# Performance work log

Measured on AMD Instinct MI355X. Metric: run time of the kernel, lower is better.

Reference implementation:

```python
import jax, jax.numpy as jnp
import numpy as np

B, N_ATOMS = 64, 127            # graphs, atoms per graph (uniform)
L = N_ATOMS + 1                 # +1 cls token
D_MODEL, NHEAD, NUM_LAYERS, D_FF = 1024, 16, 8, 3072
HEAD_DIM = D_MODEL // NHEAD
MAX_TOKENS = 131                # 121 + 10
NEIGH_VOCAB = 14 + 3            # max_neighbors + 3
DIST_VOCAB = 83 + 3             # max_distance + 3
EPS = 1e-5


def _dist_bins():
    # short_cutoff=0.9, long_cutoff=5.0, precision=0.05; first 3 edges overridden
    b = np.arange(0.9 - 3 * 0.05, 5.0, 0.05)
    b[:3] = [-1.0, 0.0, 0.01]
    return jnp.asarray(b, jnp.float32)  # len 85 -> digitize indices in [0, 85]


def _layer_norm(x, g, b):
    m = jnp.mean(x, -1, keepdims=True)
    v = jnp.var(x, -1, keepdims=True)
    return (x - m) * jax.lax.rsqrt(v + EPS) * g + b


def setup_inputs() -> dict:
    key = jax.random.key(0)
    ks = jax.random.split(key, 16)
    s = 0.02
    z = jax.random.randint(ks[0], (B * N_ATOMS,), 0, 119)
    hgs = jax.random.randint(ks[1], (B * N_ATOMS,), 0, 15)
    pos = jax.random.normal(ks[2], (B * N_ATOMS, 3), jnp.float32) * 3.0
    batch = jnp.repeat(jnp.arange(B, dtype=jnp.int64), N_ATOMS)
    atoms_emb = (jax.random.normal(ks[3], (MAX_TOKENS, D_MODEL), jnp.float32) * s).at[0].set(0.0)  # padding_idx=0
    neigh_emb = (jax.random.normal(ks[4], (NEIGH_VOCAB, D_MODEL), jnp.float32) * s).at[0].set(0.0)
    dist_emb = jax.random.normal(ks[5], (DIST_VOCAB, NHEAD), jnp.float32) * s  # row 0 forced to -inf in reference
    Wqkv = jax.random.normal(ks[6], (D_MODEL, 3 * D_MODEL), jnp.float32) * s
    bqkv = jnp.zeros((3 * D_MODEL,), jnp.float32)
    Wo = jax.random.normal(ks[7], (D_MODEL, D_MODEL), jnp.float32) * s
    bo = jnp.zeros((D_MODEL,), jnp.float32)
    W1 = jax.random.normal(ks[8], (D_MODEL, D_FF), jnp.float32) * s
    b1f = jnp.zeros((D_FF,), jnp.float32)
    W2 = jax.random.normal(ks[9], (D_FF, D_MODEL), jnp.float32) * s
    b2f = jnp.zeros((D_MODEL,), jnp.float32)
    ln1_g = jnp.ones((D_MODEL,), jnp.float32); ln1_b = jnp.zeros((D_MODEL,), jnp.float32)
    ln2_g = jnp.ones((D_MODEL,), jnp.float32); ln2_b = jnp.zeros((D_MODEL,), jnp.float32)
    return dict(z=z, hgs=hgs, pos=pos, batch=batch, atoms_emb=atoms_emb, neigh_emb=neigh_emb,
                dist_emb=dist_emb, Wqkv=Wqkv, bqkv=bqkv, Wo=Wo, bo=bo,
                W1=W1, b1f=b1f, W2=W2, b2f=b2f,
                ln1_g=ln1_g, ln1_b=ln1_b, ln2_g=ln2_g, ln2_b=ln2_b)


def reference(z, hgs, pos, batch, atoms_emb, neigh_emb, dist_emb,
              Wqkv, bqkv, Wo, bo, W1, b1f, W2, b2f, ln1_g, ln1_b, ln2_g, ln2_b):
    # batch is uniform (N_ATOMS per graph, sorted), so per-graph batching == reshape
    zb = z.reshape(B, N_ATOMS).astype(jnp.int32) + 2
    hb = hgs.reshape(B, N_ATOMS).astype(jnp.int32) + 2
    atoms = jnp.concatenate([jnp.ones((B, 1), jnp.int32), zb], axis=1)        # cls token = 1
    neighbors = jnp.concatenate([jnp.zeros((B, 1), jnp.int32), hb], axis=1)   # cls neighbors = 0

    p = pos.reshape(B, N_ATOMS, 3)
    dist = jnp.sqrt(jnp.sum((p[:, None, :, :] - p[:, :, None, :]) ** 2, axis=-1))  # (B,n,n)
    didx = jnp.digitize(dist, _dist_bins()).astype(jnp.int32)                      # self-loop -> 2
    distances = jnp.ones((B, L, L), jnp.int32).at[:, 1:, 1:].set(didx)             # cls row/col = 1

    # neg_inf_idx=0 padding mask row (unused here since no padding -> indices >= 1)
    w_d = dist_emb.at[0].set(-jnp.inf)
    d_mask = w_d[distances].transpose(0, 3, 1, 2)  # (B, H, L, L)

    x = atoms_emb[atoms] + neigh_emb[neighbors]    # (B, L, D)
    scale = 1.0 / jnp.sqrt(jnp.float32(HEAD_DIM))
    for _ in range(NUM_LAYERS):  # shared weights + shared attention bias
        qkv = x @ Wqkv + bqkv
        q, k, v = jnp.split(qkv, 3, axis=-1)
        q = q.reshape(B, L, NHEAD, HEAD_DIM)
        k = k.reshape(B, L, NHEAD, HEAD_DIM)
        v = v.reshape(B, L, NHEAD, HEAD_DIM)
        scores = jnp.einsum('blhd,bmhd->bhlm', q, k) * scale + d_mask
        a = jax.nn.softmax(scores, axis=-1)
        o = jnp.einsum('bhlm,bmhd->blhd', a, v).reshape(B, L, D_MODEL) @ Wo + bo
        x = _layer_norm(x + o, ln1_g, ln1_b)                      # post-norm (norm_first=False)
        h = jax.nn.gelu(x @ W1 + b1f, approximate=False) @ W2 + b2f
        x = _layer_norm(x + h, ln2_g, ln2_b)
    return x[:, 0]  # cls embedding, (B, D_MODEL)
```

## Files before the change

### kernel.cpp

```cpp
#include <hip/hip_runtime.h>
#include <cstdint>
#include <math.h>

typedef unsigned short u16;
typedef __attribute__((ext_vector_type(4))) float f32x4;
typedef __attribute__((ext_vector_type(8))) __bf16 bf16x8;
typedef __attribute__((ext_vector_type(8))) short short8;

typedef __attribute__((address_space(1))) void g_void;
typedef __attribute__((address_space(3))) void l_void;

__device__ __forceinline__ u16 f2bf(float f) {
  uint32_t u = __builtin_bit_cast(uint32_t, f);
  u += 0x7FFFu + ((u >> 16) & 1u);
  return (u16)(u >> 16);
}
__device__ __forceinline__ float bf2f(u16 h) {
  uint32_t u = ((uint32_t)h) << 16;
  return __builtin_bit_cast(float, u);
}

__device__ __forceinline__ void gload16(const void* g, void* l) {
  __builtin_amdgcn_global_load_lds((g_void*)g, (l_void*)l, 16, 0, 0);
}

__device__ __forceinline__ float gelu_exact(float x) {
  float a = x * 0.70710678118654752f;
  float s = fabsf(a);
  float t = __builtin_amdgcn_rcpf(fmaf(0.3275911f, s, 1.0f));
  float p = fmaf(fmaf(fmaf(fmaf(1.061405429f, t, -1.453152027f), t, 1.421413741f), t,
                      -0.284496736f), t, 0.254829592f);
  p *= t;
  float e = __expf(-s * s);
  float er = fmaf(-p, e, 1.0f);
  er = copysignf(er, a);
  return 0.5f * x * (1.0f + er);
}

__global__ void transpose_w(const float* __restrict__ W, u16* __restrict__ Wt, int K, int N) {
  __shared__ float t[32][33];
  const int nb = blockIdx.x * 32, kb = blockIdx.y * 32;
  const int tx = threadIdx.x, ty = threadIdx.y;
#pragma unroll
  for (int i = 0; i < 32; i += 8)
    t[ty + i][tx] = W[(size_t)(kb + ty + i) * N + nb + tx];
  __syncthreads();
#pragma unroll
  for (int i = 0; i < 32; i += 8)
    Wt[(size_t)(nb + ty + i) * K + kb + tx] = f2bf(t[tx][ty + i]);
}

__global__ void embed_k(const int* __restrict__ z, const int* __restrict__ hgs,
                        const float* __restrict__ ae, const float* __restrict__ ne,
                        u16* __restrict__ xb) {
  const int row = blockIdx.x;
  const int b = row >> 7, tl = row & 127;
  int ia = 1, in_ = 0;
  if (tl > 0) { ia = z[b * 127 + tl - 1] + 2; in_ = hgs[b * 127 + tl - 1] + 2; }
  const float* ar = ae + (size_t)ia * 1024;
  const float* nr = ne + (size_t)in_ * 1024;
  for (int c = threadIdx.x; c < 1024; c += 256)
    xb[(size_t)row * 1024 + c] = f2bf(ar[c] + nr[c]);
}

__global__ void mask_k(const float* __restrict__ pos, const float* __restrict__ demb,
                       u16* __restrict__ mask) {
  __shared__ float edges[85];
  __shared__ float dh[86 * 16];
  const int bq = blockIdx.x;
  const int b = bq >> 7, lq = bq & 127;
  const int lk = threadIdx.x;
  if (lk < 85) {
    double e = 0.75 + 0.05 * (double)lk;
    float ef = (float)e;
    if (lk == 0) ef = -1.0f; else if (lk == 1) ef = 0.0f; else if (lk == 2) ef = 0.01f;
    edges[lk] = ef;
  }
  for (int i = lk; i < 86 * 16; i += 128) {
    float v = demb[i];
    if (i < 16) v = -INFINITY;
    dh[i] = v;
  }
  __syncthreads();
  int c;
  if (lq == 0 || lk == 0) {
    c = 1;
  } else {
    const float* pi = pos + ((size_t)b * 127 + lq - 1) * 3;
    const float* pj = pos + ((size_t)b * 127 + lk - 1) * 3;
    const float dx = pi[0] - pj[0], dy = pi[1] - pj[1], dz = pi[2] - pj[2];
    const float d = sqrtf(dx * dx + dy * dy + dz * dz);
    int cnt = 0;
#pragma unroll
    for (int k2 = 0; k2 < 85; ++k2) cnt += (edges[k2] <= d) ? 1 : 0;
    c = cnt;
  }
#pragma unroll
  for (int h = 0; h < 16; ++h)
    mask[(((size_t)b * 16 + h) * 128 + lq) * 128 + lk] = f2bf(dh[c * 16 + h]);
}

template <int MODE, int RT>
__launch_bounds__(256, 2)
__global__ void gemmP(const u16* __restrict__ A, const u16* __restrict__ Bt,
                      const float* __restrict__ bias,
                      u16* __restrict__ O0, u16* __restrict__ O1, u16* __restrict__ O2,
                      int N, int K) {
  extern __shared__ char lds[];
  constexpr int BM = 128 * RT;
  constexpr int ASZ = 8192 * RT;
  constexpr int SLAB = ASZ + 8192;
  const int tid = threadIdx.x;
  const int w = tid >> 6, l = tid & 63;
  const int wr = w >> 1, wc = w & 1;
  const int nwg = gridDim.x;
  const int wg = (blockIdx.x & 7) * (nwg >> 3) + (blockIdx.x >> 3);
  const int ntn = N >> 7;
  const int bm = wg / ntn, bn = wg % ntn;
  const int NT = K >> 5;

  const int r15 = l >> 2;
  const int colc = ((((l & 3) << 4) ^ ((r15 & 8) << 2)) >> 1);
  const u16* Ag = A + (size_t)(bm * BM + w * 16 + r15) * K + colc;
  const u16* Bg = Bt + (size_t)(bn * 128 + w * 16 + r15) * K + colc;
  const int ldst = w << 10;

  auto stage = [&](int t, char* buf) {
    const int kb = t << 5;
#pragma unroll
    for (int c = 0; c < 2 * RT; ++c)
      gload16(Ag + (size_t)(c * 64) * K + kb, buf + c * 4096 + ldst);
#pragma unroll
    for (int c = 0; c < 2; ++c)
      gload16(Bg + (size_t)(c * 64) * K + kb, buf + ASZ + c * 4096 + ldst);
  };

  const int lo = ((l & 15) << 6) + (((l >> 4) << 4) ^ ((l & 8) << 2));

  f32x4 acc[4 * RT][4];
#pragma unroll
  for (int m = 0; m < 4 * RT; ++m)
#pragma unroll
    for (int n = 0; n < 4; ++n) acc[m][n] = f32x4{0.f, 0.f, 0.f, 0.f};

  char* p0 = lds;
  char* p1 = lds + SLAB;
  char* p2 = lds + 2 * SLAB;

  stage(0, p0);
  stage(1, p1);
  if constexpr (RT == 2) asm volatile("s_waitcnt vmcnt(6)" ::: "memory");
  else                   asm volatile("s_waitcnt vmcnt(4)" ::: "memory");
  __builtin_amdgcn_s_barrier();

  for (int t = 0; t < NT; ++t) {
    if (t + 2 < NT) stage(t + 2, p2);
    const char* ab = p0 + wr * (RT * 4096);
    const char* bb = p0 + ASZ + (wc << 12);
    bf16x8 af[4 * RT], bf[4];
#pragma unroll
    for (int m = 0; m < 4 * RT; ++m) af[m] = *(const bf16x8*)(ab + (m << 10) + lo);
#pragma unroll
    for (int n = 0; n < 4; ++n) bf[n] = *(const bf16x8*)(bb + (n << 10) + lo);
    __builtin_amdgcn_s_setprio(1);
#pragma unroll
    for (int m = 0; m < 4 * RT; ++m)
#pragma unroll
      for (int n = 0; n < 4; ++n)
        acc[m][n] = __builtin_amdgcn_mfma_f32_16x16x32_bf16(af[m], bf[n], acc[m][n], 0, 0, 0);
    __builtin_amdgcn_s_setprio(0);
    if (t + 2 < NT) {
      if constexpr (RT == 2) asm volatile("s_waitcnt vmcnt(6)" ::: "memory");
      else                   asm volatile("s_waitcnt vmcnt(4)" ::: "memory");
    } else {
      asm volatile("s_waitcnt vmcnt(0)" ::: "memory");
    }
    __builtin_amdgcn_s_barrier();
    char* tmp = p0; p0 = p1; p1 = p2; p2 = tmp;
  }

  const int fr = l & 15, fq = l >> 4;
  const int colb = bn * 128 + wc * 64;
  const int rowb = bm * BM + wr * (64 * RT);
  float bv[4];
#pragma unroll
  for (int n = 0; n < 4; ++n) bv[n] = bias[colb + n * 16 + fr];
  const int region = colb >> 10;

#pragma unroll
  for (int m = 0; m < 4 * RT; ++m) {
#pragma unroll
    for (int n = 0; n < 4; ++n) {
      const int col = colb + n * 16 + fr;
      if (MODE == 0 && region == 2) {
        const int row0_ = rowb + m * 16 + fq * 4;
        const int bI = row0_ >> 7, tl0 = row0_ & 127;
        const int c = col & 1023, h = c >> 6, d = c & 63;
        ushort4 pk;
        pk.x = f2bf(acc[m][n][0] + bv[n]);
        pk.y = f2bf(acc[m][n][1] + bv[n]);
        pk.z = f2bf(acc[m][n][2] + bv[n]);
        pk.w = f2bf(acc[m][n][3] + bv[n]);
        *(ushort4*)&O2[(((size_t)bI * 16 + h) * 64 + d) * 128 + tl0] = pk;
      } else {
#pragma unroll
        for (int j = 0; j < 4; ++j) {
          const int row = rowb + m * 16 + fq * 4 + j;
          float v = acc[m][n][j] + bv[n];
          if (MODE == 2) v = gelu_exact(v);
          if (MODE == 0) {
            const int bI = row >> 7, tl = row & 127;
            const int c = col & 1023, h = c >> 6, d = c & 63;
            if (region == 0) O0[(((size_t)bI * 16 + h) * 128 + tl) * 64 + d] = f2bf(v);
            else             O1[(((size_t)bI * 16 + h) * 128 + tl) * 64 + d] = f2bf(v);
          } else {
            O0[(size_t)row * N + col] = f2bf(v);
          }
        }
      }
    }
  }
}

__launch_bounds__(256)
__global__ void attn_kernel(const u16* __restrict__ Qg, const u16* __restrict__ Kg,
                            const u16* __restrict__ Vg,
                            const u16* __restrict__ mask,
                            u16* __restrict__ Og) {
  __shared__ u16 QK[2 * 128 * 64];
  __shared__ u16 Vt[64 * 128];
  const int tid = threadIdx.x;
  const int wv = tid >> 6;
  const int l = tid & 63;
  const int bh = blockIdx.x;
  const int b = bh >> 4;

  const char* Qs = (const char*)(Qg + (size_t)bh * 8192);
  const char* Ks = (const char*)(Kg + (size_t)bh * 8192);
  const char* Vs = (const char*)(Vg + (size_t)bh * 8192);
  char* QKb = (char*)QK;
  char* Vtb = (char*)Vt;
#pragma unroll
  for (int it = 0; it < 4; ++it) {
    const int r = it * 32 + (tid >> 3);
    const int cb = (tid & 7) * 16;
    const int sw = cb ^ ((r & 7) << 4);
    *(uint4*)(QKb + r * 128 + sw) = *(const uint4*)(Qs + r * 128 + cb);
    *(uint4*)(QKb + 16384 + r * 128 + sw) = *(const uint4*)(Ks + r * 128 + cb);
  }
#pragma unroll
  for (int it = 0; it < 4; ++it) {
    const int r = it * 16 + (tid >> 4);
    const int cb = (tid & 15) * 16;
    const int sw = cb ^ ((r & 7) << 4);
    *(uint4*)(Vtb + r * 256 + sw) = *(const uint4*)(Vs + r * 256 + cb);
  }
  __syncthreads();

  f32x4 s[2][8];
#pragma unroll
  for (int m = 0; m < 2; ++m)
#pragma unroll
    for (int n = 0; n < 8; ++n) s[m][n] = f32x4{0.f, 0.f, 0.f, 0.f};
#pragma unroll
  for (int kk = 0; kk < 2; ++kk) {
    bf16x8 qa[2], kb[8];
#pragma unroll
    for (int m = 0; m < 2; ++m) {
      const int qr = wv * 32 + m * 16 + (l & 15);
      qa[m] = *(const bf16x8*)(QKb + qr * 128 + ((kk * 64 + (l >> 4) * 16) ^ ((qr & 7) << 4)));
    }
#pragma unroll
    for (int n = 0; n < 8; ++n) {
      const int kr = n * 16 + (l & 15);
      kb[n] = *(const bf16x8*)(QKb + 16384 + kr * 128 + ((kk * 64 + (l >> 4) * 16) ^ ((kr & 7) << 4)));
    }
#pragma unroll
    for (int m = 0; m < 2; ++m)
#pragma unroll
      for (int n = 0; n < 8; ++n)
        s[m][n] = __builtin_amdgcn_mfma_f32_16x16x32_bf16(qa[m], kb[n], s[m][n], 0, 0, 0);
  }

  const u16* mbase = mask + (size_t)bh * 16384;
  float rinv[2][4];
#pragma unroll
  for (int m = 0; m < 2; ++m) {
#pragma unroll
    for (int j = 0; j < 4; ++j) {
      const int lq = wv * 32 + m * 16 + (l >> 4) * 4 + j;
      const u16* mrow = mbase + lq * 128 + (l & 15);
      float vals[8];
#pragma unroll
      for (int n = 0; n < 8; ++n)
        vals[n] = fmaf(s[m][n][j], 0.125f, bf2f(mrow[n * 16]));
      float mx = vals[0];
#pragma unroll
      for (int n = 1; n < 8; ++n) mx = fmaxf(mx, vals[n]);
#pragma unroll
      for (int o = 1; o < 16; o <<= 1) mx = fmaxf(mx, __shfl_xor(mx, o, 64));
      float sum = 0.f;
#pragma unroll
      for (int n = 0; n < 8; ++n) { vals[n] = expf(vals[n] - mx); sum += vals[n]; }
#pragma unroll
      for (int o = 1; o < 16; o <<= 1) sum += __shfl_xor(sum, o, 64);
      rinv[m][j] = 1.f / sum;
#pragma unroll
      for (int n = 0; n < 8; ++n) s[m][n][j] = vals[n];
    }
  }
  __syncthreads();
  char* Pb = QKb + wv * 8192;
#pragma unroll
  for (int m = 0; m < 2; ++m)
#pragma unroll
    for (int n = 0; n < 8; ++n)
#pragma unroll
      for (int j = 0; j < 4; ++j) {
        const int pr = m * 16 + (l >> 4) * 4 + j;
        const int pc = (n * 16 + (l & 15)) * 2;
        *(u16*)(Pb + pr * 256 + (pc ^ ((pr & 7) << 4))) = f2bf(s[m][n][j]);
      }
  __syncthreads();

  f32x4 o_[2][4];
#pragma unroll
  for (int m = 0; m < 2; ++m)
#pragma unroll
    for (int n = 0; n < 4; ++n) o_[m][n] = f32x4{0.f, 0.f, 0.f, 0.f};
#pragma unroll
  for (int ks = 0; ks < 4; ++ks) {
    bf16x8 pa[2], vb[4];
#pragma unroll
    for (int m = 0; m < 2; ++m) {
      const int pr = m * 16 + (l & 15);
      pa[m] = *(const bf16x8*)(Pb + pr * 256 + ((ks * 64 + (l >> 4) * 16) ^ ((pr & 7) << 4)));
    }
#pragma unroll
    for (int n = 0; n < 4; ++n) {
      const int vr = n * 16 + (l & 15);
      vb[n] = *(const bf16x8*)(Vtb + vr * 256 + ((ks * 64 + (l >> 4) * 16) ^ ((vr & 7) << 4)));
    }
#pragma unroll
    for (int m = 0; m < 2; ++m)
#pragma unroll
      for (int n = 0; n < 4; ++n)
        o_[m][n] = __builtin_amdgcn_mfma_f32_16x16x32_bf16(pa[m], vb[n], o_[m][n], 0, 0, 0);
  }
  const int h = bh & 15;
#pragma unroll
  for (int m = 0; m < 2; ++m)
#pragma unroll
    for (int n = 0; n < 4; ++n)
#pragma unroll
      for (int j = 0; j < 4; ++j) {
        const int lo2 = wv * 32 + m * 16 + (l >> 4) * 4 + j;
        const int d = n * 16 + (l & 15);
        Og[((size_t)b * 128 + lo2) * 1024 + h * 64 + d] = f2bf(o_[m][n][j] * rinv[m][j]);
      }
}

__launch_bounds__(256)
__global__ void ln_res(u16* __restrict__ xb, const u16* __restrict__ o,
                       const float* __restrict__ gam, const float* __restrict__ bet,
                       float* __restrict__ cls_out) {
  const int row = blockIdx.x * 4 + (threadIdx.x >> 6);
  const int l = threadIdx.x & 63;
  const size_t base = (size_t)row * 1024 + l * 16;
  const int c0 = l * 16;
  float v[16], gv[16], bb[16];
  float s = 0.f, sq = 0.f;
  const short8 xa = *(const short8*)(xb + base);
  const short8 xc = *(const short8*)(xb + base + 8);
  const short8 oa = *(const short8*)(o + base);
  const short8 oc = *(const short8*)(o + base + 8);
#pragma unroll
  for (int i = 0; i < 4; ++i) {
    *(float4*)&gv[i * 4] = *(const float4*)(gam + c0 + i * 4);
    *(float4*)&bb[i * 4] = *(const float4*)(bet + c0 + i * 4);
  }
#pragma unroll
  for (int i = 0; i < 8; ++i) {
    v[i] = bf2f((u16)xa[i]) + bf2f((u16)oa[i]);
    v[i + 8] = bf2f((u16)xc[i]) + bf2f((u16)oc[i]);
  }
#pragma unroll
  for (int i = 0; i < 16; ++i) { s += v[i]; sq += v[i] * v[i]; }
#pragma unroll
  for (int off = 1; off < 64; off <<= 1) {
    s += __shfl_xor(s, off, 64);
    sq += __shfl_xor(sq, off, 64);
  }
  const float mean = s * (1.f / 1024.f);
  const float var = sq * (1.f / 1024.f) - mean * mean;
  const float rstd = rsqrtf(var + 1e-5f);
  short8 ra, rc;
#pragma unroll
  for (int i = 0; i < 8; ++i) {
    const float ya = (v[i] - mean) * rstd * gv[i] + bb[i];
    const float yc = (v[i + 8] - mean) * rstd * gv[i + 8] + bb[i + 8];
    ra[i] = (short)f2bf(ya);
    rc[i] = (short)f2bf(yc);
    if ((row & 127) == 0) {
      cls_out[(size_t)(row >> 7) * 1024 + c0 + i] = ya;
      cls_out[(size_t)(row >> 7) * 1024 + c0 + 8 + i] = yc;
    }
  }
  *(short8*)(xb + base) = ra;
  *(short8*)(xb + base + 8) = rc;
}

extern "C" void kernel_launch(void* const* d_in, const int* in_sizes, int n_in,
                              void* d_out, int out_size, void* d_ws, size_t ws_size,
                              hipStream_t stream) {
  const int* z = (const int*)d_in[0];
  const int* hgs = (const int*)d_in[1];
  const float* pos = (const float*)d_in[2];
  const float* atoms_emb = (const float*)d_in[4];
  const float* neigh_emb = (const float*)d_in[5];
  const float* dist_emb = (const float*)d_in[6];
  const float* Wqkv = (const float*)d_in[7];
  const float* bqkv = (const float*)d_in[8];
  const float* Wo = (const float*)d_in[9];
  const float* bo = (const float*)d_in[10];
  const float* W1 = (const float*)d_in[11];
  const float* b1f = (const float*)d_in[12];
  const float* W2 = (const float*)d_in[13];
  const float* b2f = (const float*)d_in[14];
  const float* ln1g = (const float*)d_in[15];
  const float* ln1b = (const float*)d_in[16];
  const float* ln2g = (const float*)d_in[17];
  const float* ln2b = (const float*)d_in[18];

  size_t off = 0;
  char* wsb = (char*)d_ws;
  auto alc = [&](size_t bytes) { void* p = wsb + off; off += (bytes + 255) & ~(size_t)255; return p; };
  u16* xb = (u16*)alc(8192ull * 1024 * 2);
  u16* q = (u16*)alc(8192ull * 1024 * 2);
  u16* k = (u16*)alc(8192ull * 1024 * 2);
  u16* v = (u16*)alc(8192ull * 1024 * 2);
  u16* big = (u16*)alc(8192ull * 3072 * 2);
  u16* proj = (u16*)alc(8192ull * 1024 * 2);
  u16* wqkvt = (u16*)alc(3072ull * 1024 * 2);
  u16* wot = (u16*)alc(1024ull * 1024 * 2);
  u16* w1t = (u16*)alc(3072ull * 1024 * 2);
  u16* w2t = (u16*)alc(1024ull * 3072 * 2);
  u16* mask = (u16*)alc(64ull * 16 * 128 * 128 * 2);

  hipFuncSetAttribute((const void*)gemmP<0, 2>, hipFuncAttributeMaxDynamicSharedMemorySize, 73728);
  hipFuncSetAttribute((const void*)gemmP<2, 2>, hipFuncAttributeMaxDynamicSharedMemorySize, 73728);
  hipFuncSetAttribute((const void*)gemmP<1, 1>, hipFuncAttributeMaxDynamicSharedMemorySize, 49152);

  transpose_w<<<dim3(96, 32), dim3(32, 8), 0, stream>>>(Wqkv, wqkvt, 1024, 3072);
  transpose_w<<<dim3(32, 32), dim3(32, 8), 0, stream>>>(Wo, wot, 1024, 1024);
  transpose_w<<<dim3(96, 32), dim3(32, 8), 0, stream>>>(W1, w1t, 1024, 3072);
  transpose_w<<<dim3(32, 96), dim3(32, 8), 0, stream>>>(W2, w2t, 3072, 1024);
  embed_k<<<8192, 256, 0, stream>>>(z, hgs, atoms_emb, neigh_emb, xb);
  mask_k<<<8192, 128, 0, stream>>>(pos, dist_emb, mask);

  float* cls = (float*)d_out;
  for (int layer = 0; layer < 8; ++layer) {
    gemmP<0, 2><<<768, 256, 73728, stream>>>(xb, wqkvt, bqkv, q, k, v, 3072, 1024);
    attn_kernel<<<1024, 256, 0, stream>>>(q, k, v, mask, big);
    gemmP<1, 1><<<512, 256, 49152, stream>>>(big, wot, bo, proj, nullptr, nullptr, 1024, 1024);
    ln_res<<<2048, 256, 0, stream>>>(xb, proj, ln1g, ln1b, cls);
    gemmP<2, 2><<<768, 256, 73728, stream>>>(xb, w1t, b1f, big, nullptr, nullptr, 3072, 1024);
    gemmP<1, 1><<<512, 256, 49152, stream>>>(big, w2t, b2f, proj, nullptr, nullptr, 1024, 3072);
    ln_res<<<2048, 256, 0, stream>>>(xb, proj, ln2g, ln2b, cls);
  }
}
```

Baseline: 2.382 ms.

## Use 512-thread 256x128 GEMM tiles and split-K for N=1024 GEMMs, fusing reduction into LayerNorm

Replaces the templated GEMM with a 512-thread, 8-wave kernel in which every GEMM uses 256x128 tiles and each wave computes a 64x64 sub-tile. The two N=1024 GEMMs (output projection and FFN down-projection) are split along K into two halves that write fp32 partials. The residual LayerNorm kernel now sums both partials, adds the bias and applies the residual and normalization. The aim is better data reuse per tile, and enough blocks for the narrow GEMMs without the earlier 128-row tiles. The cost is extra fp32 partial-sum traffic, which is aliased onto the q/k/v/proj workspace.

```diff
diff --git a/kernel.cpp b/kernel.cpp
--- a/kernel.cpp
+++ b/kernel.cpp
@@ -100,46 +100,44 @@
     mask[(((size_t)b * 16 + h) * 128 + lq) * 128 + lk] = f2bf(dh[c * 16 + h]);
 }
 
-template <int MODE, int RT>
-__launch_bounds__(256, 2)
-__global__ void gemmP(const u16* __restrict__ A, const u16* __restrict__ Bt,
+template <int MODE>
+__launch_bounds__(512, 4)
+__global__ void gemmS(const u16* __restrict__ A, const u16* __restrict__ Bt,
                       const float* __restrict__ bias,
                       u16* __restrict__ O0, u16* __restrict__ O1, u16* __restrict__ O2,
-                      int N, int K) {
+                      float* __restrict__ Pout,
+                      int N, int K, int ntiles, int kLen) {
   extern __shared__ char lds[];
-  constexpr int BM = 128 * RT;
-  constexpr int ASZ = 8192 * RT;
-  constexpr int SLAB = ASZ + 8192;
+  constexpr int SLAB = 24576;
   const int tid = threadIdx.x;
   const int w = tid >> 6, l = tid & 63;
   const int wr = w >> 1, wc = w & 1;
   const int nwg = gridDim.x;
   const int wg = (blockIdx.x & 7) * (nwg >> 3) + (blockIdx.x >> 3);
+  const int s = wg / ntiles;
+  const int tile = wg - s * ntiles;
   const int ntn = N >> 7;
-  const int bm = wg / ntn, bn = wg % ntn;
-  const int NT = K >> 5;
-
-  const int r15 = l >> 2;
-  const int colc = ((((l & 3) << 4) ^ ((r15 & 8) << 2)) >> 1);
-  const u16* Ag = A + (size_t)(bm * BM + w * 16 + r15) * K + colc;
-  const u16* Bg = Bt + (size_t)(bn * 128 + w * 16 + r15) * K + colc;
+  const int bm = tile / ntn, bn = tile - (tile / ntn) * ntn;
+  const int kStart = s * kLen;
+  const int NT = kLen >> 5;
+
+  const int colc = ((((l & 3) << 4) ^ (((l >> 2) & 8) << 2)) >> 1);
+  const u16* Ag = A + (size_t)(bm * 256 + w * 16 + (l >> 2)) * K + kStart + colc;
+  const u16* Bg = Bt + (size_t)(bn * 128 + w * 16 + (l >> 2)) * K + kStart + colc;
   const int ldst = w << 10;
 
   auto stage = [&](int t, char* buf) {
     const int kb = t << 5;
-#pragma unroll
-    for (int c = 0; c < 2 * RT; ++c)
-      gload16(Ag + (size_t)(c * 64) * K + kb, buf + c * 4096 + ldst);
-#pragma unroll
-    for (int c = 0; c < 2; ++c)
-      gload16(Bg + (size_t)(c * 64) * K + kb, buf + ASZ + c * 4096 + ldst);
+    gload16(Ag + kb, buf + ldst);
+    gload16(Ag + (size_t)128 * K + kb, buf + 8192 + ldst);
+    gload16(Bg + kb, buf + 16384 + ldst);
   };
 
   const int lo = ((l & 15) << 6) + (((l >> 4) << 4) ^ ((l & 8) << 2));
 
-  f32x4 acc[4 * RT][4];
-#pragma unroll
-  for (int m = 0; m < 4 * RT; ++m)
+  f32x4 acc[4][4];
+#pragma unroll
+  for (int m = 0; m < 4; ++m)
 #pragma unroll
     for (int n = 0; n < 4; ++n) acc[m][n] = f32x4{0.f, 0.f, 0.f, 0.f};
 
@@ -149,46 +147,43 @@
 
   stage(0, p0);
   stage(1, p1);
-  if constexpr (RT == 2) asm volatile("s_waitcnt vmcnt(6)" ::: "memory");
-  else                   asm volatile("s_waitcnt vmcnt(4)" ::: "memory");
+  asm volatile("s_waitcnt vmcnt(3)" ::: "memory");
   __builtin_amdgcn_s_barrier();
 
   for (int t = 0; t < NT; ++t) {
     if (t + 2 < NT) stage(t + 2, p2);
-    const char* ab = p0 + wr * (RT * 4096);
-    const char* bb = p0 + ASZ + (wc << 12);
-    bf16x8 af[4 * RT], bf[4];
-#pragma unroll
-    for (int m = 0; m < 4 * RT; ++m) af[m] = *(const bf16x8*)(ab + (m << 10) + lo);
+    const char* ab = p0 + (wr << 12);
+    const char* bb = p0 + 16384 + (wc << 12);
+    bf16x8 af[4], bf[4];
+#pragma unroll
+    for (int m = 0; m < 4; ++m) af[m] = *(const bf16x8*)(ab + (m << 10) + lo);
 #pragma unroll
     for (int n = 0; n < 4; ++n) bf[n] = *(const bf16x8*)(bb + (n << 10) + lo);
     __builtin_amdgcn_s_setprio(1);
 #pragma unroll
-    for (int m = 0; m < 4 * RT; ++m)
+    for (int m = 0; m < 4; ++m)
 #pragma unroll
       for (int n = 0; n < 4; ++n)
         acc[m][n] = __builtin_amdgcn_mfma_f32_16x16x32_bf16(af[m], bf[n], acc[m][n], 0, 0, 0);
     __builtin_amdgcn_s_setprio(0);
-    if (t + 2 < NT) {
-      if constexpr (RT == 2) asm volatile("s_waitcnt vmcnt(6)" ::: "memory");
-      else                   asm volatile("s_waitcnt vmcnt(4)" ::: "memory");
-    } else {
-      asm volatile("s_waitcnt vmcnt(0)" ::: "memory");
-    }
+    if (t + 2 < NT) asm volatile("s_waitcnt vmcnt(3)" ::: "memory");
+    else            asm volatile("s_waitcnt vmcnt(0)" ::: "memory");
     __builtin_amdgcn_s_barrier();
     char* tmp = p0; p0 = p1; p1 = p2; p2 = tmp;
   }
 
   const int fr = l & 15, fq = l >> 4;
   const int colb = bn * 128 + wc * 64;
-  const int rowb = bm * BM + wr * (64 * RT);
+  const int rowb = bm * 256 + wr * 64;
   float bv[4];
-#pragma unroll
-  for (int n = 0; n < 4; ++n) bv[n] = bias[colb + n * 16 + fr];
+  if (MODE != 3) {
+#pragma unroll
+    for (int n = 0; n < 4; ++n) bv[n] = bias[colb + n * 16 + fr];
+  }
   const int region = colb >> 10;
 
 #pragma unroll
-  for (int m = 0; m < 4 * RT; ++m) {
+  for (int m = 0; m < 4; ++m) {
 #pragma unroll
     for (int n = 0; n < 4; ++n) {
       const int col = colb + n * 16 + fr;
@@ -206,15 +201,19 @@
 #pragma unroll
         for (int j = 0; j < 4; ++j) {
           const int row = rowb + m * 16 + fq * 4 + j;
-          float v = acc[m][n][j] + bv[n];
-          if (MODE == 2) v = gelu_exact(v);
-          if (MODE == 0) {
-            const int bI = row >> 7, tl = row & 127;
-            const int c = col & 1023, h = c >> 6, d = c & 63;
-            if (region == 0) O0[(((size_t)bI * 16 + h) * 128 + tl) * 64 + d] = f2bf(v);
-            else             O1[(((size_t)bI * 16 + h) * 128 + tl) * 64 + d] = f2bf(v);
+          if (MODE == 3) {
+            Pout[(size_t)s * 8388608 + (size_t)row * N + col] = acc[m][n][j];
           } else {
-            O0[(size_t)row * N + col] = f2bf(v);
+            float v = acc[m][n][j] + bv[n];
+            if (MODE == 2) v = gelu_exact(v);
+            if (MODE == 0) {
+              const int bI = row >> 7, tl = row & 127;
+              const int c = col & 1023, h = c >> 6, d = c & 63;
+              if (region == 0) O0[(((size_t)bI * 16 + h) * 128 + tl) * 64 + d] = f2bf(v);
+              else             O1[(((size_t)bI * 16 + h) * 128 + tl) * 64 + d] = f2bf(v);
+            } else {
+              O0[(size_t)row * N + col] = f2bf(v);
+            }
           }
         }
       }
@@ -361,28 +360,30 @@
 }
 
 __launch_bounds__(256)
-__global__ void ln_res(u16* __restrict__ xb, const u16* __restrict__ o,
-                       const float* __restrict__ gam, const float* __restrict__ bet,
-                       float* __restrict__ cls_out) {
+__global__ void ln_resS(u16* __restrict__ xb, const float* __restrict__ P,
+                        const float* __restrict__ bias,
+                        const float* __restrict__ gam, const float* __restrict__ bet,
+                        float* __restrict__ cls_out) {
   const int row = blockIdx.x * 4 + (threadIdx.x >> 6);
   const int l = threadIdx.x & 63;
   const size_t base = (size_t)row * 1024 + l * 16;
   const int c0 = l * 16;
-  float v[16], gv[16], bb[16];
-  float s = 0.f, sq = 0.f;
+  float v[16], gv[16], bb[16], bi[16], pa[16], pb[16];
   const short8 xa = *(const short8*)(xb + base);
   const short8 xc = *(const short8*)(xb + base + 8);
-  const short8 oa = *(const short8*)(o + base);
-  const short8 oc = *(const short8*)(o + base + 8);
 #pragma unroll
   for (int i = 0; i < 4; ++i) {
+    *(float4*)&pa[i * 4] = *(const float4*)(P + base + i * 4);
+    *(float4*)&pb[i * 4] = *(const float4*)(P + 8388608 + base + i * 4);
     *(float4*)&gv[i * 4] = *(const float4*)(gam + c0 + i * 4);
     *(float4*)&bb[i * 4] = *(const float4*)(bet + c0 + i * 4);
-  }
+    *(float4*)&bi[i * 4] = *(const float4*)(bias + c0 + i * 4);
+  }
+  float s = 0.f, sq = 0.f;
 #pragma unroll
   for (int i = 0; i < 8; ++i) {
-    v[i] = bf2f((u16)xa[i]) + bf2f((u16)oa[i]);
-    v[i + 8] = bf2f((u16)xc[i]) + bf2f((u16)oc[i]);
+    v[i] = bf2f((u16)xa[i]) + pa[i] + pb[i] + bi[i];
+    v[i + 8] = bf2f((u16)xc[i]) + pa[i + 8] + pb[i + 8] + bi[i + 8];
   }
 #pragma unroll
   for (int i = 0; i < 16; ++i) { s += v[i]; sq += v[i] * v[i]; }
@@ -439,17 +440,19 @@
   u16* q = (u16*)alc(8192ull * 1024 * 2);
   u16* k = (u16*)alc(8192ull * 1024 * 2);
   u16* v = (u16*)alc(8192ull * 1024 * 2);
+  u16* proj = (u16*)alc(8192ull * 1024 * 2);
   u16* big = (u16*)alc(8192ull * 3072 * 2);
-  u16* proj = (u16*)alc(8192ull * 1024 * 2);
   u16* wqkvt = (u16*)alc(3072ull * 1024 * 2);
   u16* wot = (u16*)alc(1024ull * 1024 * 2);
   u16* w1t = (u16*)alc(3072ull * 1024 * 2);
   u16* w2t = (u16*)alc(1024ull * 3072 * 2);
   u16* mask = (u16*)alc(64ull * 16 * 128 * 128 * 2);
-
-  hipFuncSetAttribute((const void*)gemmP<0, 2>, hipFuncAttributeMaxDynamicSharedMemorySize, 73728);
-  hipFuncSetAttribute((const void*)gemmP<2, 2>, hipFuncAttributeMaxDynamicSharedMemorySize, 73728);
-  hipFuncSetAttribute((const void*)gemmP<1, 1>, hipFuncAttributeMaxDynamicSharedMemorySize, 49152);
+  float* pp = (float*)q;
+  (void)proj;
+
+  hipFuncSetAttribute((const void*)gemmS<0>, hipFuncAttributeMaxDynamicSharedMemorySize, 73728);
+  hipFuncSetAttribute((const void*)gemmS<2>, hipFuncAttributeMaxDynamicSharedMemorySize, 73728);
+  hipFuncSetAttribute((const void*)gemmS<3>, hipFuncAttributeMaxDynamicSharedMemorySize, 73728);
 
   transpose_w<<<dim3(96, 32), dim3(32, 8), 0, stream>>>(Wqkv, wqkvt, 1024, 3072);
   transpose_w<<<dim3(32, 32), dim3(32, 8), 0, stream>>>(Wo, wot, 1024, 1024);
@@ -460,12 +463,12 @@
 
   float* cls = (float*)d_out;
   for (int layer = 0; layer < 8; ++layer) {
-    gemmP<0, 2><<<768, 256, 73728, stream>>>(xb, wqkvt, bqkv, q, k, v, 3072, 1024);
+    gemmS<0><<<768, 512, 73728, stream>>>(xb, wqkvt, bqkv, q, k, v, nullptr, 3072, 1024, 768, 1024);
     attn_kernel<<<1024, 256, 0, stream>>>(q, k, v, mask, big);
-    gemmP<1, 1><<<512, 256, 49152, stream>>>(big, wot, bo, proj, nullptr, nullptr, 1024, 1024);
-    ln_res<<<2048, 256, 0, stream>>>(xb, proj, ln1g, ln1b, cls);
-    gemmP<2, 2><<<768, 256, 73728, stream>>>(xb, w1t, b1f, big, nullptr, nullptr, 3072, 1024);
-    gemmP<1, 1><<<512, 256, 49152, stream>>>(big, w2t, b2f, proj, nullptr, nullptr, 1024, 3072);
-    ln_res<<<2048, 256, 0, stream>>>(xb, proj, ln2g, ln2b, cls);
-  }
-}
+    gemmS<3><<<512, 512, 73728, stream>>>(big, wot, nullptr, nullptr, nullptr, nullptr, pp, 1024, 1024, 256, 512);
+    ln_resS<<<2048, 256, 0, stream>>>(xb, pp, bo, ln1g, ln1b, cls);
+    gemmS<2><<<768, 512, 73728, stream>>>(xb, w1t, b1f, big, nullptr, nullptr, nullptr, 3072, 1024, 768, 1024);
+    gemmS<3><<<512, 512, 73728, stream>>>(big, w2t, nullptr, nullptr, nullptr, nullptr, pp, 1024, 3072, 256, 1536);
+    ln_resS<<<2048, 256, 0, stream>>>(xb, pp, b2f, ln2g, ln2b, cls);
+  }
+}
```

Result: faster. 2.315 ms (-2.8%).

## Use 128x128 GEMM tiles at higher occupancy and vectorize the attention-mask layout

Applied to the files above, without the earlier changes.

Replaces the templated GEMM with a single 128x128-tile variant for all projections, using 48KB of LDS and launch bounds of three blocks per CU, which doubles the grid for the N=3072 GEMMs. The distance-bias mask is stored in an interleaved layout so each attention row reads its eight bias values with one 16-byte load instead of eight strided scalar loads. A __syncthreads between the P write and the PV stage in attention is removed, on the assumption that each wave touches only its own LDS slice. Smaller tiles give less data reuse per block in exchange for more blocks in flight and better latency hiding.

```diff
diff --git a/kernel.cpp b/kernel.cpp
--- a/kernel.cpp
+++ b/kernel.cpp
@@ -95,51 +95,47 @@
     for (int k2 = 0; k2 < 85; ++k2) cnt += (edges[k2] <= d) ? 1 : 0;
     c = cnt;
   }
+  const int fr = lk & 15, nn = lk >> 4;
 #pragma unroll
   for (int h = 0; h < 16; ++h)
-    mask[(((size_t)b * 16 + h) * 128 + lq) * 128 + lk] = f2bf(dh[c * 16 + h]);
-}
-
-template <int MODE, int RT>
-__launch_bounds__(256, 2)
-__global__ void gemmP(const u16* __restrict__ A, const u16* __restrict__ Bt,
+    mask[((((size_t)(b * 16 + h) * 16 + fr) * 128 + lq) << 3) + nn] = f2bf(dh[c * 16 + h]);
+}
+
+template <int MODE>
+__launch_bounds__(256, 3)
+__global__ void gemm4(const u16* __restrict__ A, const u16* __restrict__ Bt,
                       const float* __restrict__ bias,
                       u16* __restrict__ O0, u16* __restrict__ O1, u16* __restrict__ O2,
                       int N, int K) {
   extern __shared__ char lds[];
-  constexpr int BM = 128 * RT;
-  constexpr int ASZ = 8192 * RT;
-  constexpr int SLAB = ASZ + 8192;
+  constexpr int SLAB = 16384;
   const int tid = threadIdx.x;
   const int w = tid >> 6, l = tid & 63;
   const int wr = w >> 1, wc = w & 1;
   const int nwg = gridDim.x;
   const int wg = (blockIdx.x & 7) * (nwg >> 3) + (blockIdx.x >> 3);
   const int ntn = N >> 7;
-  const int bm = wg / ntn, bn = wg % ntn;
+  const int bm = wg / ntn, bn = wg - (wg / ntn) * ntn;
   const int NT = K >> 5;
 
-  const int r15 = l >> 2;
-  const int colc = ((((l & 3) << 4) ^ ((r15 & 8) << 2)) >> 1);
-  const u16* Ag = A + (size_t)(bm * BM + w * 16 + r15) * K + colc;
-  const u16* Bg = Bt + (size_t)(bn * 128 + w * 16 + r15) * K + colc;
+  const int colc = ((((l & 3) << 4) ^ (((l >> 2) & 8) << 2)) >> 1);
+  const u16* Ag = A + (size_t)(bm * 128 + w * 16 + (l >> 2)) * K + colc;
+  const u16* Bg = Bt + (size_t)(bn * 128 + w * 16 + (l >> 2)) * K + colc;
   const int ldst = w << 10;
 
   auto stage = [&](int t, char* buf) {
     const int kb = t << 5;
-#pragma unroll
-    for (int c = 0; c < 2 * RT; ++c)
-      gload16(Ag + (size_t)(c * 64) * K + kb, buf + c * 4096 + ldst);
-#pragma unroll
-    for (int c = 0; c < 2; ++c)
-      gload16(Bg + (size_t)(c * 64) * K + kb, buf + ASZ + c * 4096 + ldst);
+    gload16(Ag + kb, buf + ldst);
+    gload16(Ag + (size_t)64 * K + kb, buf + 4096 + ldst);
+    gload16(Bg + kb, buf + 8192 + ldst);
+    gload16(Bg + (size_t)64 * K + kb, buf + 12288 + ldst);
   };
 
   const int lo = ((l & 15) << 6) + (((l >> 4) << 4) ^ ((l & 8) << 2));
 
-  f32x4 acc[4 * RT][4];
-#pragma unroll
-  for (int m = 0; m < 4 * RT; ++m)
+  f32x4 acc[4][4];
+#pragma unroll
+  for (int m = 0; m < 4; ++m)
 #pragma unroll
     for (int n = 0; n < 4; ++n) acc[m][n] = f32x4{0.f, 0.f, 0.f, 0.f};
 
@@ -149,46 +145,41 @@
 
   stage(0, p0);
   stage(1, p1);
-  if constexpr (RT == 2) asm volatile("s_waitcnt vmcnt(6)" ::: "memory");
-  else                   asm volatile("s_waitcnt vmcnt(4)" ::: "memory");
+  asm volatile("s_waitcnt vmcnt(4)" ::: "memory");
   __builtin_amdgcn_s_barrier();
 
   for (int t = 0; t < NT; ++t) {
     if (t + 2 < NT) stage(t + 2, p2);
-    const char* ab = p0 + wr * (RT * 4096);
-    const char* bb = p0 + ASZ + (wc << 12);
-    bf16x8 af[4 * RT], bf[4];
-#pragma unroll
-    for (int m = 0; m < 4 * RT; ++m) af[m] = *(const bf16x8*)(ab + (m << 10) + lo);
+    const char* ab = p0 + (wr << 12);
+    const char* bb = p0 + 8192 + (wc << 12);
+    bf16x8 af[4], bf[4];
+#pragma unroll
+    for (int m = 0; m < 4; ++m) af[m] = *(const bf16x8*)(ab + (m << 10) + lo);
 #pragma unroll
     for (int n = 0; n < 4; ++n) bf[n] = *(const bf16x8*)(bb + (n << 10) + lo);
     __builtin_amdgcn_s_setprio(1);
 #pragma unroll
-    for (int m = 0; m < 4 * RT; ++m)
+    for (int m = 0; m < 4; ++m)
 #pragma unroll
       for (int n = 0; n < 4; ++n)
         acc[m][n] = __builtin_amdgcn_mfma_f32_16x16x32_bf16(af[m], bf[n], acc[m][n], 0, 0, 0);
     __builtin_amdgcn_s_setprio(0);
-    if (t + 2 < NT) {
-      if constexpr (RT == 2) asm volatile("s_waitcnt vmcnt(6)" ::: "memory");
-      else                   asm volatile("s_waitcnt vmcnt(4)" ::: "memory");
-    } else {
-      asm volatile("s_waitcnt vmcnt(0)" ::: "memory");
-    }
+    if (t + 2 < NT) asm volatile("s_waitcnt vmcnt(4)" ::: "memory");
+    else            asm volatile("s_waitcnt vmcnt(0)" ::: "memory");
     __builtin_amdgcn_s_barrier();
     char* tmp = p0; p0 = p1; p1 = p2; p2 = tmp;
   }
 
   const int fr = l & 15, fq = l >> 4;
   const int colb = bn * 128 + wc * 64;
-  const int rowb = bm * BM + wr * (64 * RT);
+  const int rowb = bm * 128 + wr * 64;
   float bv[4];
 #pragma unroll
   for (int n = 0; n < 4; ++n) bv[n] = bias[colb + n * 16 + fr];
   const int region = colb >> 10;
 
 #pragma unroll
-  for (int m = 0; m < 4 * RT; ++m) {
+  for (int m = 0; m < 4; ++m) {
 #pragma unroll
     for (int n = 0; n < 4; ++n) {
       const int col = colb + n * 16 + fr;
@@ -282,18 +273,18 @@
         s[m][n] = __builtin_amdgcn_mfma_f32_16x16x32_bf16(qa[m], kb[n], s[m][n], 0, 0, 0);
   }
 
-  const u16* mbase = mask + (size_t)bh * 16384;
+  const u16* mb2 = mask + (((size_t)bh * 16 + (l & 15)) << 10);
   float rinv[2][4];
 #pragma unroll
   for (int m = 0; m < 2; ++m) {
 #pragma unroll
     for (int j = 0; j < 4; ++j) {
       const int lq = wv * 32 + m * 16 + (l >> 4) * 4 + j;
-      const u16* mrow = mbase + lq * 128 + (l & 15);
+      const short8 mv = *(const short8*)(mb2 + lq * 8);
       float vals[8];
 #pragma unroll
       for (int n = 0; n < 8; ++n)
-        vals[n] = fmaf(s[m][n][j], 0.125f, bf2f(mrow[n * 16]));
+        vals[n] = fmaf(s[m][n][j], 0.125f, bf2f((u16)mv[n]));
       float mx = vals[0];
 #pragma unroll
       for (int n = 1; n < 8; ++n) mx = fmaxf(mx, vals[n]);
@@ -321,7 +312,6 @@
         const int pc = (n * 16 + (l & 15)) * 2;
         *(u16*)(Pb + pr * 256 + (pc ^ ((pr & 7) << 4))) = f2bf(s[m][n][j]);
       }
-  __syncthreads();
 
   f32x4 o_[2][4];
 #pragma unroll
@@ -369,7 +359,6 @@
   const size_t base = (size_t)row * 1024 + l * 16;
   const int c0 = l * 16;
   float v[16], gv[16], bb[16];
-  float s = 0.f, sq = 0.f;
   const short8 xa = *(const short8*)(xb + base);
   const short8 xc = *(const short8*)(xb + base + 8);
   const short8 oa = *(const short8*)(o + base);
@@ -379,6 +368,7 @@
     *(float4*)&gv[i * 4] = *(const float4*)(gam + c0 + i * 4);
     *(float4*)&bb[i * 4] = *(const float4*)(bet + c0 + i * 4);
   }
+  float s = 0.f, sq = 0.f;
 #pragma unroll
   for (int i = 0; i < 8; ++i) {
     v[i] = bf2f((u16)xa[i]) + bf2f((u16)oa[i]);
@@ -439,17 +429,17 @@
   u16* q = (u16*)alc(8192ull * 1024 * 2);
   u16* k = (u16*)alc(8192ull * 1024 * 2);
   u16* v = (u16*)alc(8192ull * 1024 * 2);
+  u16* proj = (u16*)alc(8192ull * 1024 * 2);
   u16* big = (u16*)alc(8192ull * 3072 * 2);
-  u16* proj = (u16*)alc(8192ull * 1024 * 2);
   u16* wqkvt = (u16*)alc(3072ull * 1024 * 2);
   u16* wot = (u16*)alc(1024ull * 1024 * 2);
   u16* w1t = (u16*)alc(3072ull * 1024 * 2);
   u16* w2t = (u16*)alc(1024ull * 3072 * 2);
-  u16* mask = (u16*)alc(64ull * 16 * 128 * 128 * 2);
-
-  hipFuncSetAttribute((const void*)gemmP<0, 2>, hipFuncAttributeMaxDynamicSharedMemorySize, 73728);
-  hipFuncSetAttribute((const void*)gemmP<2, 2>, hipFuncAttributeMaxDynamicSharedMemorySize, 73728);
-  hipFuncSetAttribute((const void*)gemmP<1, 1>, hipFuncAttributeMaxDynamicSharedMemorySize, 49152);
+  u16* mask = (u16*)alc(64ull * 16 * 16 * 128 * 8 * 2);
+
+  hipFuncSetAttribute((const void*)gemm4<0>, hipFuncAttributeMaxDynamicSharedMemorySize, 49152);
+  hipFuncSetAttribute((const void*)gemm4<1>, hipFuncAttributeMaxDynamicSharedMemorySize, 49152);
+  hipFuncSetAttribute((const void*)gemm4<2>, hipFuncAttributeMaxDynamicSharedMemorySize, 49152);
 
   transpose_w<<<dim3(96, 32), dim3(32, 8), 0, stream>>>(Wqkv, wqkvt, 1024, 3072);
   transpose_w<<<dim3(32, 32), dim3(32, 8), 0, stream>>>(Wo, wot, 1024, 1024);
@@ -460,12 +450,12 @@
 
   float* cls = (float*)d_out;
   for (int layer = 0; layer < 8; ++layer) {
-    gemmP<0, 2><<<768, 256, 73728, stream>>>(xb, wqkvt, bqkv, q, k, v, 3072, 1024);
+    gemm4<0><<<1536, 256, 49152, stream>>>(xb, wqkvt, bqkv, q, k, v, 3072, 1024);
     attn_kernel<<<1024, 256, 0, stream>>>(q, k, v, mask, big);
-    gemmP<1, 1><<<512, 256, 49152, stream>>>(big, wot, bo, proj, nullptr, nullptr, 1024, 1024);
+    gemm4<1><<<512, 256, 49152, stream>>>(big, wot, bo, proj, nullptr, nullptr, 1024, 1024);
     ln_res<<<2048, 256, 0, stream>>>(xb, proj, ln1g, ln1b, cls);
-    gemmP<2, 2><<<768, 256, 73728, stream>>>(xb, w1t, b1f, big, nullptr, nullptr, 3072, 1024);
-    gemmP<1, 1><<<512, 256, 49152, stream>>>(big, w2t, b2f, proj, nullptr, nullptr, 1024, 3072);
+    gemm4<2><<<1536, 256, 49152, stream>>>(xb, w1t, b1f, big, nullptr, nullptr, 3072, 1024);
+    gemm4<1><<<512, 256, 49152, stream>>>(big, w2t, b2f, proj, nullptr, nullptr, 1024, 3072);
     ln_res<<<2048, 256, 0, stream>>>(xb, proj, ln2g, ln2b, cls);
   }
 }
```

New measurement: 2.292 ms. 1.04x faster.
